# Performance work log

Hardware: AMD Instinct MI355X
Metric: run time of the kernel (lower is better)

Reference implementation:

```python
import jax, jax.numpy as jnp
import numpy as np

K = 5  # kernel_size (odd -> 'same' output size given the pad in semi_conv)
B, C_IN, C_OUT, H, W = 4, 8, 16, 192, 192
NEG_INF = -jnp.inf  # aggregation identity of the (max, +) semifield


def setup_inputs() -> dict:
    key = jax.random.key(0)
    kx, ks = jax.random.split(key)
    x = jax.random.normal(kx, (B, C_IN, H, W), dtype=jnp.float32)
    # torch.rand((C_out, C_in)) -> uniform(0,1); lower-bounded at 0.25 to avoid
    # numerically extreme kernels from near-zero scales (division by 4*scale).
    scales = jax.random.uniform(ks, (C_OUT, C_IN), dtype=jnp.float32, minval=0.25, maxval=1.0)
    return {"x": x, "scales": scales}


def _compute_kernel(scales):
    # matches torch.linspace(-K//2 + 1, K//2, K) with Python floor division
    start = (-K) // 2 + 1
    z_i = jnp.linspace(float(start), float(K // 2), K, dtype=jnp.float32)
    z = z_i[:, None] ** 2 + z_i[None, :] ** 2                  # [K, K]
    return -z[None, None, :, :] / (4.0 * scales[:, :, None, None])  # [C_out, C_in, K, K]


def _maxplus_conv(x, w):
    # result[b,co,h,w] = sum_ci max_{i,j} ( x_pad[b,ci,h+i,w+j] + w[co,ci,i,j] )
    b, c_in, h, wd = x.shape
    c_out = w.shape[0]
    p = K // 2
    xp = jnp.pad(x, ((0, 0), (0, 0), (p, p), (p, p)), constant_values=NEG_INF)
    # running max over the K*K kernel offsets; avoids the [B,Co,Ci,K*K,H*W] unfold blow-up
    acc = jnp.full((b, c_out, c_in, h, wd), NEG_INF, dtype=x.dtype)
    for i in range(K):
        for j in range(K):
            patch = xp[:, None, :, i:i + h, j:j + wd]           # [B,1,C_in,H,W]
            wij = w[None, :, :, i, j][..., None, None]          # [1,C_out,C_in,1,1]
            acc = jnp.maximum(acc, patch + wij)
    return jnp.sum(acc, axis=2)                                 # [B,C_out,H,W]


def reference(x, scales):
    return _maxplus_conv(x, _compute_kernel(scales))
```

## Files before the change

kernel.cpp:

```cpp
#include <hip/hip_runtime.h>
#include <cmath>

#define B_    4
#define CIN   8
#define COUT  16
#define H_    192
#define W_    192
#define TW    32
#define TH    16
#define SX    36
#define SY    20
#define NCO   4
#define NT    128
#define SLAB  (SY * SX)
#define NF2   (SLAB / 2)
#define CHAN_F2 (H_ * W_ / 2)

__global__ __launch_bounds__(NT, 2)
void semiconv_kernel(const float* __restrict__ x,
                     const float* __restrict__ scales,
                     float* __restrict__ out) {
    __shared__ float tile[CIN * SLAB];
    __shared__ float wtab[NCO * CIN];

    int blk = blockIdx.x;
    const int tile_x = blk % 6;  blk /= 6;
    const int tile_y = blk % 12; blk /= 12;
    const int cg     = blk & 3;  blk >>= 2;
    const int b      = blk;

    const int tid = threadIdx.x;
    const int py  = tid >> 3;
    const int p0  = (tid & 7) * 4;

    if (tid < NCO * CIN)
        wtab[tid] = 0.25f / scales[cg * NCO * CIN + tid];

    const int gy0  = tile_y * TH - 2;
    const int gxp0 = tile_x * (TW / 2) - 1;
    int gidx[3]; bool okk[3];
    {
        int e = tid;
        #pragma unroll
        for (int k = 0; k < 3; ++k) {
            int ey = e / 18, ex = e - ey * 18;
            int gy = gy0 + ey, gxp = gxp0 + ex;
            okk[k]  = (gy >= 0) && (gy < H_) && (gxp >= 0) && (gxp < W_ / 2);
            gidx[k] = gy * (W_ / 2) + gxp;
            e += NT;
        }
    }
    const bool tail = tid < (NF2 - 2 * NT);

    const float2* xb = (const float2*)(x + (size_t)b * CIN * H_ * W_);
    const float2 NEG2 = make_float2(-INFINITY, -INFINITY);
    float2 pf[CIN][3];
    #pragma unroll
    for (int ci = 0; ci < CIN; ++ci) {
        const float2* xp = xb + ci * CHAN_F2;
        pf[ci][0] = okk[0] ? xp[gidx[0]] : NEG2;
        pf[ci][1] = okk[1] ? xp[gidx[1]] : NEG2;
        pf[ci][2] = (tail && okk[2]) ? xp[gidx[2]] : NEG2;
    }
    float2* lp = (float2*)tile;
    #pragma unroll
    for (int ci = 0; ci < CIN; ++ci) {
        lp[ci * NF2 + tid]          = pf[ci][0];
        lp[ci * NF2 + tid + NT]     = pf[ci][1];
        if (tail) lp[ci * NF2 + tid + 2 * NT] = pf[ci][2];
    }

    __syncthreads();

    float wa[NCO][CIN];
    #pragma unroll
    for (int c = 0; c < NCO; ++c)
        #pragma unroll
        for (int ci = 0; ci < CIN; ++ci)
            wa[c][ci] = wtab[c * CIN + ci];

    float acc[NCO][4];
    #pragma unroll
    for (int c = 0; c < NCO; ++c)
        #pragma unroll
        for (int p = 0; p < 4; ++p) acc[c][p] = 0.f;

    const float* tb = tile + py * SX + p0;

    #pragma unroll
    for (int ci = 0; ci < CIN; ++ci) {
        const float* tp = tb + ci * SLAB;

        float X[5][8];
        #pragma unroll
        for (int r = 0; r < 5; ++r) {
            float4 lo = *(const float4*)(tp + r * SX);
            float4 hi = *(const float4*)(tp + r * SX + 4);
            X[r][0] = lo.x; X[r][1] = lo.y; X[r][2] = lo.z; X[r][3] = lo.w;
            X[r][4] = hi.x; X[r][5] = hi.y; X[r][6] = hi.z; X[r][7] = hi.w;
        }

        float V0[8], V1[8], V4[8];
        #pragma unroll
        for (int c = 0; c < 8; ++c) {
            V0[c] = X[2][c];
            V1[c] = fmaxf(X[1][c], X[3][c]);
            V4[c] = fmaxf(X[0][c], X[4][c]);
        }

        float A1[NCO], A2[NCO], A4[NCO], A5[NCO], A8[NCO];
        #pragma unroll
        for (int c = 0; c < NCO; ++c) {
            float a = wa[c][ci];
            A1[c] = a;
            A2[c] = a + a;
            A4[c] = A2[c] + A2[c];
            A5[c] = A4[c] + a;
            A8[c] = A4[c] + A4[c];
        }

        #pragma unroll
        for (int p = 0; p < 4; ++p) {
            const int c = p + 2;
            float M0 = V0[c];
            float M1 = fmaxf(fmaxf(V0[c - 1], V0[c + 1]), V1[c]);
            float M2 = fmaxf(V1[c - 1], V1[c + 1]);
            float M4 = fmaxf(fmaxf(V0[c - 2], V0[c + 2]), V4[c]);
            float M5 = fmaxf(fmaxf(V1[c - 2], V1[c + 2]),
                             fmaxf(V4[c - 1], V4[c + 1]));
            float M8 = fmaxf(V4[c - 2], V4[c + 2]);
            #pragma unroll
            for (int co = 0; co < NCO; ++co) {
                float lo3 = fmaxf(fmaxf(M1 - A1[co], M2 - A2[co]), M0);
                float hi3 = fmaxf(fmaxf(M4 - A4[co], M5 - A5[co]),
                                  M8 - A8[co]);
                acc[co][p] += fmaxf(lo3, hi3);
            }
        }
    }

    const int gy = tile_y * TH + py;
    const int gx = tile_x * TW + p0;
    #pragma unroll
    for (int co = 0; co < NCO; ++co) {
        float* op = out + ((size_t)((b * COUT + cg * NCO + co) * H_) + gy) * W_ + gx;
        *(float4*)op = make_float4(acc[co][0], acc[co][1], acc[co][2], acc[co][3]);
    }
}

extern "C" void kernel_launch(void* const* d_in, const int* in_sizes, int n_in,
                              void* d_out, int out_size, void* d_ws, size_t ws_size,
                              hipStream_t stream) {
    const float* x      = (const float*)d_in[0];
    const float* scales = (const float*)d_in[1];
    float* out          = (float*)d_out;

    const int n_blocks = B_ * (COUT / NCO) * (H_ / TH) * (W_ / TW);
    semiconv_kernel<<<n_blocks, NT, 0, stream>>>(x, scales, out);
}
```

Before: 17.70 us.

## Split input channels across two thread groups with LDS reduction

```diff
diff --git a/kernel.cpp b/kernel.cpp
--- a/kernel.cpp
+++ b/kernel.cpp
@@ -11,12 +11,12 @@
 #define SX    36
 #define SY    20
 #define NCO   4
-#define NT    128
+#define NT    256
 #define SLAB  (SY * SX)
 #define NF2   (SLAB / 2)
 #define CHAN_F2 (H_ * W_ / 2)
 
-__global__ __launch_bounds__(NT, 2)
+__global__ __launch_bounds__(NT, 4)
 void semiconv_kernel(const float* __restrict__ x,
                      const float* __restrict__ scales,
                      float* __restrict__ out) {
@@ -30,19 +30,21 @@
     const int b      = blk;
 
     const int tid = threadIdx.x;
-    const int py  = tid >> 3;
-    const int p0  = (tid & 7) * 4;
+    const int lt  = tid & 127;
+    const int grp = tid >> 7;
+    const int py  = lt >> 3;
+    const int p0  = (lt & 7) * 4;
 
     if (tid < NCO * CIN)
         wtab[tid] = 0.25f / scales[cg * NCO * CIN + tid];
 
     const int gy0  = tile_y * TH - 2;
     const int gxp0 = tile_x * (TW / 2) - 1;
-    int gidx[3]; bool okk[3];
+    int gidx[2]; bool okk[2];
     {
         int e = tid;
         #pragma unroll
-        for (int k = 0; k < 3; ++k) {
+        for (int k = 0; k < 2; ++k) {
             int ey = e / 18, ex = e - ey * 18;
             int gy = gy0 + ey, gxp = gxp0 + ex;
             okk[k]  = (gy >= 0) && (gy < H_) && (gxp >= 0) && (gxp < W_ / 2);
@@ -50,34 +52,32 @@
             e += NT;
         }
     }
-    const bool tail = tid < (NF2 - 2 * NT);
+    const bool tail = tid < (NF2 - NT);
 
     const float2* xb = (const float2*)(x + (size_t)b * CIN * H_ * W_);
     const float2 NEG2 = make_float2(-INFINITY, -INFINITY);
-    float2 pf[CIN][3];
+    float2 pf[CIN][2];
     #pragma unroll
     for (int ci = 0; ci < CIN; ++ci) {
         const float2* xp = xb + ci * CHAN_F2;
         pf[ci][0] = okk[0] ? xp[gidx[0]] : NEG2;
-        pf[ci][1] = okk[1] ? xp[gidx[1]] : NEG2;
-        pf[ci][2] = (tail && okk[2]) ? xp[gidx[2]] : NEG2;
+        pf[ci][1] = (tail && okk[1]) ? xp[gidx[1]] : NEG2;
     }
     float2* lp = (float2*)tile;
     #pragma unroll
     for (int ci = 0; ci < CIN; ++ci) {
-        lp[ci * NF2 + tid]          = pf[ci][0];
-        lp[ci * NF2 + tid + NT]     = pf[ci][1];
-        if (tail) lp[ci * NF2 + tid + 2 * NT] = pf[ci][2];
+        lp[ci * NF2 + tid] = pf[ci][0];
+        if (tail) lp[ci * NF2 + tid + NT] = pf[ci][1];
     }
 
     __syncthreads();
 
-    float wa[NCO][CIN];
+    float wa[NCO][4];
     #pragma unroll
     for (int c = 0; c < NCO; ++c)
         #pragma unroll
-        for (int ci = 0; ci < CIN; ++ci)
-            wa[c][ci] = wtab[c * CIN + ci];
+        for (int k = 0; k < 4; ++k)
+            wa[c][k] = wtab[c * CIN + grp * 4 + k];
 
     float acc[NCO][4];
     #pragma unroll
@@ -85,11 +85,11 @@
         #pragma unroll
         for (int p = 0; p < 4; ++p) acc[c][p] = 0.f;
 
-    const float* tb = tile + py * SX + p0;
+    const float* tb = tile + grp * 4 * SLAB + py * SX + p0;
 
     #pragma unroll
-    for (int ci = 0; ci < CIN; ++ci) {
-        const float* tp = tb + ci * SLAB;
+    for (int k = 0; k < 4; ++k) {
+        const float* tp = tb + k * SLAB;
 
         float X[5][8];
         #pragma unroll
@@ -111,7 +111,7 @@
         float A1[NCO], A2[NCO], A4[NCO], A5[NCO], A8[NCO];
         #pragma unroll
         for (int c = 0; c < NCO; ++c) {
-            float a = wa[c][ci];
+            float a = wa[c][k];
             A1[c] = a;
             A2[c] = a + a;
             A4[c] = A2[c] + A2[c];
@@ -139,12 +139,25 @@
         }
     }
 
-    const int gy = tile_y * TH + py;
-    const int gx = tile_x * TW + p0;
-    #pragma unroll
-    for (int co = 0; co < NCO; ++co) {
-        float* op = out + ((size_t)((b * COUT + cg * NCO + co) * H_) + gy) * W_ + gx;
-        *(float4*)op = make_float4(acc[co][0], acc[co][1], acc[co][2], acc[co][3]);
+    float* cbuf = tile + 4 * SLAB;
+    if (grp == 1) {
+        float4* cb = (float4*)(cbuf + lt * 16);
+        #pragma unroll
+        for (int co = 0; co < NCO; ++co)
+            cb[co] = make_float4(acc[co][0], acc[co][1], acc[co][2], acc[co][3]);
+    }
+    __syncthreads();
+    if (grp == 0) {
+        const float4* cb = (const float4*)(cbuf + lt * 16);
+        const int gy = tile_y * TH + py;
+        const int gx = tile_x * TW + p0;
+        #pragma unroll
+        for (int co = 0; co < NCO; ++co) {
+            float4 o = cb[co];
+            float* op = out + ((size_t)((b * COUT + cg * NCO + co) * H_) + gy) * W_ + gx;
+            *(float4*)op = make_float4(acc[co][0] + o.x, acc[co][1] + o.y,
+                                       acc[co][2] + o.z, acc[co][3] + o.w);
+        }
     }
 }
 
```

New measurement: 16.95 us. 1.04x faster.

## Compute all output channels per block with 16x16 tiles and packed float2 math

Applied to the files above, without the earlier changes.

```diff
diff --git a/kernel.cpp b/kernel.cpp
--- a/kernel.cpp
+++ b/kernel.cpp
@@ -1,150 +1,142 @@
 #include <hip/hip_runtime.h>
 #include <cmath>
+
+typedef float v2f __attribute__((ext_vector_type(2)));
 
 #define B_    4
 #define CIN   8
 #define COUT  16
 #define H_    192
 #define W_    192
-#define TW    32
-#define TH    16
-#define SX    36
-#define SY    20
-#define NCO   4
+#define T_    16
+#define SXc   20
+#define SYc   20
+#define SLAB  (SYc * SXc)
+#define NF2   (SLAB / 2)
 #define NT    128
-#define SLAB  (SY * SX)
-#define NF2   (SLAB / 2)
 #define CHAN_F2 (H_ * W_ / 2)
 
-__global__ __launch_bounds__(NT, 2)
+__global__ __launch_bounds__(NT, 4)
 void semiconv_kernel(const float* __restrict__ x,
                      const float* __restrict__ scales,
                      float* __restrict__ out) {
-    __shared__ float tile[CIN * SLAB];
-    __shared__ float wtab[NCO * CIN];
+    __shared__ __align__(16) float tile[CIN * SLAB];
+    __shared__ __align__(16) float wtab[CIN][COUT];
 
     int blk = blockIdx.x;
-    const int tile_x = blk % 6;  blk /= 6;
+    const int tile_x = blk % 12; blk /= 12;
     const int tile_y = blk % 12; blk /= 12;
-    const int cg     = blk & 3;  blk >>= 2;
     const int b      = blk;
 
     const int tid = threadIdx.x;
     const int py  = tid >> 3;
-    const int p0  = (tid & 7) * 4;
+    const int q   = tid & 7;
 
-    if (tid < NCO * CIN)
-        wtab[tid] = 0.25f / scales[cg * NCO * CIN + tid];
+    {
+        const int ci = tid >> 4, co = tid & 15;
+        wtab[ci][co] = 0.25f / scales[co * CIN + ci];
+    }
 
-    const int gy0  = tile_y * TH - 2;
-    const int gxp0 = tile_x * (TW / 2) - 1;
-    int gidx[3]; bool okk[3];
-    {
-        int e = tid;
-        #pragma unroll
-        for (int k = 0; k < 3; ++k) {
-            int ey = e / 18, ex = e - ey * 18;
-            int gy = gy0 + ey, gxp = gxp0 + ex;
-            okk[k]  = (gy >= 0) && (gy < H_) && (gxp >= 0) && (gxp < W_ / 2);
-            gidx[k] = gy * (W_ / 2) + gxp;
-            e += NT;
-        }
+    const int gy0  = tile_y * T_ - 2;
+    const int gxp0 = tile_x * (T_ / 2) - 1;
+    int gidx[2]; bool okk[2];
+    #pragma unroll
+    for (int k = 0; k < 2; ++k) {
+        const int e  = tid + k * NT;
+        const int ey = e / 10, ex = e - ey * 10;
+        const int gy = gy0 + ey, gxp = gxp0 + ex;
+        okk[k]  = (gy >= 0) && (gy < H_) && (gxp >= 0) && (gxp < W_ / 2);
+        gidx[k] = gy * (W_ / 2) + gxp;
     }
-    const bool tail = tid < (NF2 - 2 * NT);
+    const bool tail = tid < (NF2 - NT);
 
     const float2* xb = (const float2*)(x + (size_t)b * CIN * H_ * W_);
     const float2 NEG2 = make_float2(-INFINITY, -INFINITY);
-    float2 pf[CIN][3];
+    float2 pf[CIN][2];
     #pragma unroll
     for (int ci = 0; ci < CIN; ++ci) {
         const float2* xp = xb + ci * CHAN_F2;
         pf[ci][0] = okk[0] ? xp[gidx[0]] : NEG2;
-        pf[ci][1] = okk[1] ? xp[gidx[1]] : NEG2;
-        pf[ci][2] = (tail && okk[2]) ? xp[gidx[2]] : NEG2;
+        pf[ci][1] = (tail && okk[1]) ? xp[gidx[1]] : NEG2;
     }
     float2* lp = (float2*)tile;
     #pragma unroll
     for (int ci = 0; ci < CIN; ++ci) {
-        lp[ci * NF2 + tid]          = pf[ci][0];
-        lp[ci * NF2 + tid + NT]     = pf[ci][1];
-        if (tail) lp[ci * NF2 + tid + 2 * NT] = pf[ci][2];
+        lp[ci * NF2 + tid] = pf[ci][0];
+        if (tail) lp[ci * NF2 + tid + NT] = pf[ci][1];
     }
 
     __syncthreads();
 
-    float wa[NCO][CIN];
+    v2f acc[COUT];
     #pragma unroll
-    for (int c = 0; c < NCO; ++c)
-        #pragma unroll
-        for (int ci = 0; ci < CIN; ++ci)
-            wa[c][ci] = wtab[c * CIN + ci];
+    for (int co = 0; co < COUT; ++co) acc[co] = (v2f){0.f, 0.f};
 
-    float acc[NCO][4];
-    #pragma unroll
-    for (int c = 0; c < NCO; ++c)
-        #pragma unroll
-        for (int p = 0; p < 4; ++p) acc[c][p] = 0.f;
-
-    const float* tb = tile + py * SX + p0;
+    const float* tb = tile + py * SXc + 2 * q;
 
     #pragma unroll
     for (int ci = 0; ci < CIN; ++ci) {
         const float* tp = tb + ci * SLAB;
 
-        float X[5][8];
+        float X[5][6];
         #pragma unroll
         for (int r = 0; r < 5; ++r) {
-            float4 lo = *(const float4*)(tp + r * SX);
-            float4 hi = *(const float4*)(tp + r * SX + 4);
-            X[r][0] = lo.x; X[r][1] = lo.y; X[r][2] = lo.z; X[r][3] = lo.w;
-            X[r][4] = hi.x; X[r][5] = hi.y; X[r][6] = hi.z; X[r][7] = hi.w;
+            v2f xa = *(const v2f*)(tp + r * SXc);
+            v2f xm = *(const v2f*)(tp + r * SXc + 2);
+            v2f xc = *(const v2f*)(tp + r * SXc + 4);
+            X[r][0] = xa.x; X[r][1] = xa.y;
+            X[r][2] = xm.x; X[r][3] = xm.y;
+            X[r][4] = xc.x; X[r][5] = xc.y;
         }
 
-        float V0[8], V1[8], V4[8];
+        float V0[6], V1[6], V4[6];
         #pragma unroll
-        for (int c = 0; c < 8; ++c) {
+        for (int c = 0; c < 6; ++c) {
             V0[c] = X[2][c];
             V1[c] = fmaxf(X[1][c], X[3][c]);
             V4[c] = fmaxf(X[0][c], X[4][c]);
         }
 
-        float A1[NCO], A2[NCO], A4[NCO], A5[NCO], A8[NCO];
-        #pragma unroll
-        for (int c = 0; c < NCO; ++c) {
-            float a = wa[c][ci];
-            A1[c] = a;
-            A2[c] = a + a;
-            A4[c] = A2[c] + A2[c];
-            A5[c] = A4[c] + a;
-            A8[c] = A4[c] + A4[c];
-        }
+        v2f M0 = (v2f){V0[2], V0[3]};
+        v2f M1 = (v2f){fmaxf(fmaxf(V0[1], V0[3]), V1[2]),
+                       fmaxf(fmaxf(V0[2], V0[4]), V1[3])};
+        v2f M2 = (v2f){fmaxf(V1[1], V1[3]),
+                       fmaxf(V1[2], V1[4])};
+        v2f M4 = (v2f){fmaxf(fmaxf(V0[0], V0[4]), V4[2]),
+                       fmaxf(fmaxf(V0[1], V0[5]), V4[3])};
+        v2f M5 = (v2f){fmaxf(fmaxf(V1[0], V1[4]), fmaxf(V4[1], V4[3])),
+                       fmaxf(fmaxf(V1[1], V1[5]), fmaxf(V4[2], V4[4]))};
+        v2f M8 = (v2f){fmaxf(V4[0], V4[4]),
+                       fmaxf(V4[1], V4[5])};
+
+        const float4* wr = (const float4*)&wtab[ci][0];
+        const float4 w0 = wr[0], w1 = wr[1], w2 = wr[2], w3 = wr[3];
 
         #pragma unroll
-        for (int p = 0; p < 4; ++p) {
-            const int c = p + 2;
-            float M0 = V0[c];
-            float M1 = fmaxf(fmaxf(V0[c - 1], V0[c + 1]), V1[c]);
-            float M2 = fmaxf(V1[c - 1], V1[c + 1]);
-            float M4 = fmaxf(fmaxf(V0[c - 2], V0[c + 2]), V4[c]);
-            float M5 = fmaxf(fmaxf(V1[c - 2], V1[c + 2]),
-                             fmaxf(V4[c - 1], V4[c + 1]));
-            float M8 = fmaxf(V4[c - 2], V4[c + 2]);
-            #pragma unroll
-            for (int co = 0; co < NCO; ++co) {
-                float lo3 = fmaxf(fmaxf(M1 - A1[co], M2 - A2[co]), M0);
-                float hi3 = fmaxf(fmaxf(M4 - A4[co], M5 - A5[co]),
-                                  M8 - A8[co]);
-                acc[co][p] += fmaxf(lo3, hi3);
-            }
+        for (int co = 0; co < COUT; ++co) {
+            const float4 wv = (co < 4) ? w0 : (co < 8) ? w1 : (co < 12) ? w2 : w3;
+            const float a  = (&wv.x)[co & 3];
+            const v2f aa = (v2f){a, a};
+            v2f s1 = M1 - aa;
+            v2f s2 = M2 - 2.f * aa;
+            v2f s4 = M4 - 4.f * aa;
+            v2f s5 = M5 - 5.f * aa;
+            v2f s8 = M8 - 8.f * aa;
+            v2f vm;
+            vm.x = fmaxf(fmaxf(fmaxf(s1.x, s2.x), M0.x),
+                         fmaxf(fmaxf(s4.x, s5.x), s8.x));
+            vm.y = fmaxf(fmaxf(fmaxf(s1.y, s2.y), M0.y),
+                         fmaxf(fmaxf(s4.y, s5.y), s8.y));
+            acc[co] += vm;
         }
     }
 
-    const int gy = tile_y * TH + py;
-    const int gx = tile_x * TW + p0;
+    const int gy = tile_y * T_ + py;
+    const int gx = tile_x * T_ + 2 * q;
     #pragma unroll
-    for (int co = 0; co < NCO; ++co) {
-        float* op = out + ((size_t)((b * COUT + cg * NCO + co) * H_) + gy) * W_ + gx;
-        *(float4*)op = make_float4(acc[co][0], acc[co][1], acc[co][2], acc[co][3]);
+    for (int co = 0; co < COUT; ++co) {
+        float* op = out + ((size_t)((b * COUT + co) * H_) + gy) * W_ + gx;
+        *(v2f*)op = acc[co];
     }
 }
 
@@ -155,6 +147,6 @@
     const float* scales = (const float*)d_in[1];
     float* out          = (float*)d_out;
 
-    const int n_blocks = B_ * (COUT / NCO) * (H_ / TH) * (W_ / TW);
+    const int n_blocks = B_ * (H_ / T_) * (W_ / T_);
     semiconv_kernel<<<n_blocks, NT, 0, stream>>>(x, scales, out);
 }
```

Result: no change. 17.93 us (+1.3%).
